# Optimization experiments

Hardware: AMD Instinct MI355X
Metric: run time of the kernel (lower is better)

## Reference

```python
import jax, jax.numpy as jnp
import numpy as np

D, N, M = 256, 8192, 8192
DISTANCE_THRESH = 0.8


def setup_inputs() -> dict:
    key = jax.random.key(0)
    k0, k1 = jax.random.split(key)
    d0 = jax.random.normal(k0, (D, N), dtype=jnp.float32)
    d1 = jax.random.normal(k1, (D, M), dtype=jnp.float32)
    # descriptors are L2-normalized along the feature dim (cosine similarity,
    # consistent with the 2*(1-sim) squared-distance formula in the module)
    d0 = d0 / jnp.linalg.norm(d0, axis=0, keepdims=True)
    d1 = d1 / jnp.linalg.norm(d1, axis=0, keepdims=True)
    return {"descriptors0": d0, "descriptors1": d1}


def reference(descriptors0, descriptors1):
    # nn_sim: [N, M] similarity matrix
    nn_sim = jnp.einsum('dn,dm->nm', descriptors0, descriptors1)
    nn_dist_01 = jnp.max(nn_sim, axis=1)          # [N]
    nn_idx_01 = jnp.argmax(nn_sim, axis=1)        # [N]
    nn_idx_10 = jnp.argmax(nn_sim, axis=0)        # [M]
    nn_dist = 2.0 * (1.0 - nn_dist_01)            # squared L2 dist for unit vecs
    ids1 = jnp.arange(nn_sim.shape[0])
    mask = ids1 == nn_idx_10[nn_idx_01]           # mutual NN check
    if DISTANCE_THRESH > 0.0:
        mask = mask & (nn_dist <= DISTANCE_THRESH ** 2)
    matches = jnp.where(mask, nn_idx_01, -1)
    scores = jnp.where(mask, (nn_dist + 1.0) / 2.0, 0.0)
    return matches, scores
```

## Files before the change

### kernel.cpp

```cpp
#include <hip/hip_runtime.h>
#include <hip/hip_bf16.h>

typedef __attribute__((ext_vector_type(8))) short short8;
typedef __attribute__((ext_vector_type(4))) float floatx4;
typedef unsigned int u32;

#define D_DIM 256
#define TCOLS 32
#define TILES 8
#define IDX_BITS 0x1FFFu
#define VAL_MASK 0xFFFFE000u


__device__ inline unsigned short f2bf_rne(float f) {
  u32 u = __float_as_uint(f);
  u32 r = (u + 0x7FFFu + ((u >> 16) & 1u)) >> 16;
  return (unsigned short)r;
}

__device__ inline u32 umax(u32 a, u32 b) { return a > b ? a : b; }

__device__ inline void async_ld16(const void* g, void* l) {
  __builtin_amdgcn_global_load_lds((const __attribute__((address_space(1))) void*)g,
                                   (__attribute__((address_space(3))) void*)l, 16, 0, 0);
}


__global__ __launch_bounds__(256) void transpose_cast(const float* __restrict__ src,
                                                      unsigned short* __restrict__ dst, int C,
                                                      u32* __restrict__ best, int init_n) {
  __shared__ alignas(16) unsigned short tile[64 * 132];
  const int tid = threadIdx.x;
  const int d = tid & 63;
  const int gd0 = blockIdx.x * 64;
  const int fy = blockIdx.y;
#pragma unroll
  for (int k = 0; k < 32; ++k) {
    int fl = (tid >> 6) + 4 * k;
    float v = src[(size_t)(fy * 128 + fl) * C + gd0 + d];
    tile[d * 132 + fl] = f2bf_rne(v);
  }
  __syncthreads();
#pragma unroll
  for (int c = 0; c < 4; ++c) {
    int slot = c * 256 + tid;
    int dd = slot >> 4, f8 = slot & 15;
    short8 o = *(const short8*)(tile + dd * 132 + f8 * 8);
    *(short8*)(dst + (size_t)(gd0 + dd) * D_DIM + fy * 128 + f8 * 8) = o;
  }
  if (fy == 0) {
    int i = blockIdx.x * 256 + tid;
    if (i < init_n) best[i] = 0u;
  }
}

template <bool PRECAST>
__global__ __launch_bounds__(256, 1) void gemm_reduce(const float* __restrict__ A,
                                                      const unsigned short* __restrict__ At,
                                                      const unsigned short* __restrict__ Bt,
                                                      u32* __restrict__ best01,
                                                      u32* __restrict__ best10,
                                                      int N) {
  __shared__ alignas(16) unsigned short sB[2][TCOLS * D_DIM];
  __shared__ u32 colbest[TILES * TCOLS];

  const int tid  = threadIdx.x;
  const int wave = tid >> 6;
  const int lane = tid & 63;
  const int quad = lane >> 4;
  const int l15  = lane & 15;
  const int n0   = blockIdx.x * 256;
  const int mg0  = blockIdx.y * (TILES * TCOLS);
  const int rbase = n0 + wave * 64;

  colbest[tid] = 0u;

  {
    const unsigned short* src = Bt + (size_t)mg0 * D_DIM;
#pragma unroll
    for (int c = 0; c < 4; ++c) {
      int slot = c * 256 + tid;
      int r = slot >> 5, cc = slot & 31;
      int ccg = (cc & 24) | ((cc ^ r) & 7);
      async_ld16(src + (size_t)r * D_DIM + ccg * 8, (unsigned short*)sB[0] + slot * 8);
    }
  }

  short8 af[4][8];
  if constexpr (PRECAST) {
#pragma unroll
    for (int t = 0; t < 4; ++t) {
      const unsigned short* ap = At + (size_t)(rbase + t * 16 + l15) * D_DIM + quad * 8;
#pragma unroll
      for (int kc = 0; kc < 8; ++kc)
        af[t][kc] = *(const short8*)(ap + kc * 32);
    }
  } else {
#pragma unroll
    for (int t = 0; t < 4; ++t)
#pragma unroll
      for (int kc = 0; kc < 8; ++kc) {
        const int row = rbase + t * 16 + l15;
        const int kb = kc * 32 + quad * 8;
        short8 o;
#pragma unroll
        for (int u = 0; u < 8; ++u)
          o[u] = (short)f2bf_rne(A[(size_t)(kb + u) * N + row]);
        af[t][kc] = o;
      }
  }

  u32 rbk[16];
  u32 rowpay[16];
#pragma unroll
  for (int i = 0; i < 4; ++i)
#pragma unroll
    for (int r = 0; r < 4; ++r) {
      rbk[i * 4 + r] = 0u;
      rowpay[i * 4 + r] = (~(u32)(rbase + i * 16 + quad * 4 + r)) & IDX_BITS;
    }

  __syncthreads();

  for (int mt = 0; mt < TILES; ++mt) {
    const int m0 = mg0 + mt * TCOLS;
    if (mt + 1 < TILES) {
      const unsigned short* src = Bt + (size_t)(m0 + TCOLS) * D_DIM;
      unsigned short* dstb = (unsigned short*)sB[(mt + 1) & 1];
#pragma unroll
      for (int c = 0; c < 4; ++c) {
        int slot = c * 256 + tid;
        int r = slot >> 5, cc = slot & 31;
        int ccg = (cc & 24) | ((cc ^ r) & 7);
        async_ld16(src + (size_t)r * D_DIM + ccg * 8, dstb + slot * 8);
      }
    }

    floatx4 acc[4][2];
#pragma unroll
    for (int i = 0; i < 4; ++i)
#pragma unroll
      for (int j = 0; j < 2; ++j)
        acc[i][j] = (floatx4){2.0f, 2.0f, 2.0f, 2.0f};

    const unsigned short* sb = (const unsigned short*)sB[mt & 1];
#pragma unroll
    for (int kc = 0; kc < 8; ++kc) {
      short8 bfr[2];
#pragma unroll
      for (int j = 0; j < 2; ++j) {
        int c2 = j * 16 + l15;
        int ch = kc * 4 + quad;
        int chg = (ch & 24) | ((ch ^ c2) & 7);
        bfr[j] = *(const short8*)(sb + c2 * D_DIM + chg * 8);
      }
#pragma unroll
      for (int i = 0; i < 4; ++i)
#pragma unroll
        for (int j = 0; j < 2; ++j)
          acc[i][j] = __builtin_amdgcn_mfma_f32_16x16x32_bf16(af[i][kc], bfr[j], acc[i][j], 0, 0, 0);
    }

    u32 cb[2] = {0u, 0u};
    u32 colpay[2];
#pragma unroll
    for (int j = 0; j < 2; ++j) colpay[j] = (~(u32)(m0 + j * 16 + l15)) & IDX_BITS;
#pragma unroll
    for (int i = 0; i < 4; ++i)
#pragma unroll
      for (int r = 0; r < 4; ++r) {
        u32 rp = rowpay[i * 4 + r];
        u32 rb = rbk[i * 4 + r];
#pragma unroll
        for (int j = 0; j < 2; ++j) {
          u32 u = __float_as_uint(acc[i][j][r]) & VAL_MASK;
          rb = umax(rb, u | colpay[j]);
          cb[j] = umax(cb[j], u | rp);
        }
        rbk[i * 4 + r] = rb;
      }
#pragma unroll
    for (int j = 0; j < 2; ++j) {
      u32 b = cb[j];
      b = umax(b, (u32)__shfl_xor((int)b, 16, 64));
      b = umax(b, (u32)__shfl_xor((int)b, 32, 64));
      if (quad == 0) atomicMax(&colbest[mt * TCOLS + j * 16 + l15], b);
    }
    __syncthreads();
  }

#pragma unroll
  for (int i = 0; i < 4; ++i)
#pragma unroll
    for (int r = 0; r < 4; ++r) {
      u32 b = rbk[i * 4 + r];
      b = umax(b, (u32)__shfl_xor((int)b, 1, 64));
      b = umax(b, (u32)__shfl_xor((int)b, 2, 64));
      b = umax(b, (u32)__shfl_xor((int)b, 4, 64));
      b = umax(b, (u32)__shfl_xor((int)b, 8, 64));
      if (l15 == 0) atomicMax(&best01[rbase + i * 16 + quad * 4 + r], b);
    }

  atomicMax(&best10[mg0 + tid], colbest[tid]);
}

__global__ void finalize(const u32* __restrict__ best01, const u32* __restrict__ best10,
                         float* __restrict__ out, int N) {
  int n = blockIdx.x * blockDim.x + threadIdx.x;
  if (n >= N) return;
  u32 k = best01[n];
  int idx01 = (int)((~k) & IDX_BITS);
  float sim = __uint_as_float(k & VAL_MASK) - 2.0f;
  int idx10 = (int)((~best10[idx01]) & IDX_BITS);
  float dist = 2.0f - 2.0f * sim;
  bool ok = (idx10 == n) && (dist <= 0.64f);
  out[n]     = ok ? (float)idx01 : -1.0f;
  out[N + n] = ok ? 1.5f - sim : 0.0f;
}


extern "C" void kernel_launch(void* const* d_in, const int* in_sizes, int n_in,
                              void* d_out, int out_size, void* d_ws, size_t ws_size,
                              hipStream_t stream) {
  (void)n_in; (void)out_size;
  const float* d0 = (const float*)d_in[0];
  const float* d1 = (const float*)d_in[1];
  const int N = in_sizes[0] / D_DIM;
  const int M = in_sizes[1] / D_DIM;

  u32* best01 = (u32*)d_ws;
  u32* best10 = best01 + N;
  unsigned short* At = (unsigned short*)(best10 + M);
  unsigned short* Bt = At + (size_t)N * D_DIM;
  float* out = (float*)d_out;

  const size_t need = (size_t)(N + M) * sizeof(u32) +
                      (size_t)(N + M) * D_DIM * sizeof(unsigned short);

  if (ws_size >= need) {
    hipLaunchKernelGGL(transpose_cast, dim3(N / 64, 2), dim3(256), 0, stream,
                       d0, At, N, best01, N + M);
    hipLaunchKernelGGL(transpose_cast, dim3(M / 64, 2), dim3(256), 0, stream,
                       d1, Bt, M, best01, 0);
    hipLaunchKernelGGL((gemm_reduce<true>), dim3(N / 256, M / (TILES * TCOLS)), dim3(256),
                       0, stream, d0, At, Bt, best01, best10, N);
  } else {
    unsigned short* BtF = (unsigned short*)(best10 + M);
    hipLaunchKernelGGL(transpose_cast, dim3(M / 64, 2), dim3(256), 0, stream,
                       d1, BtF, M, best01, N + M);
    hipLaunchKernelGGL((gemm_reduce<false>), dim3(N / 256, M / (TILES * TCOLS)), dim3(256),
                       0, stream, d0, BtF, BtF, best01, best10, N);
  }
  hipLaunchKernelGGL(finalize, dim3(N / 256), dim3(256), 0, stream, best01, best10, out, N);
}
```

Before: 114.1 us.

## Triple-buffer B tiles and overlap epilogue with next tile's MFMA

Switches the GEMM's B staging from double to triple buffering so two tiles are in flight, and replaces __syncthreads with explicit vmcnt waits plus s_barrier. The argmax epilogue of tile mt-1 now runs after tile mt's MFMAs, using two alternating accumulator sets, and MFMA sections are wrapped in s_setprio. The two transpose/cast launches are merged into one kernel, and row payloads are computed from a single base value to save registers. This aims to hide load latency and epilogue ALU work behind matrix ops. The cost is more LDS and a second accumulator set, which adds register pressure at one wave per SIMD.

```diff
diff --git a/kernel.cpp b/kernel.cpp
--- a/kernel.cpp
+++ b/kernel.cpp
@@ -25,14 +25,63 @@
                                    (__attribute__((address_space(3))) void*)l, 16, 0, 0);
 }
 
-
-__global__ __launch_bounds__(256) void transpose_cast(const float* __restrict__ src,
-                                                      unsigned short* __restrict__ dst, int C,
-                                                      u32* __restrict__ best, int init_n) {
+__device__ __forceinline__ void stage_tile(const unsigned short* __restrict__ src,
+                                           unsigned short* dstb, int tid) {
+#pragma unroll
+  for (int c = 0; c < 4; ++c) {
+    int slot = c * 256 + tid;
+    int r = slot >> 5, cc = slot & 31;
+    int ccg = (cc & 24) | ((cc ^ r) & 7);
+    async_ld16(src + (size_t)r * D_DIM + ccg * 8, dstb + slot * 8);
+  }
+}
+
+__device__ __forceinline__ void epilogue(const floatx4 (&acc)[4][2], int m0,
+                                         u32 (&rbk)[16], u32 rp0,
+                                         u32* __restrict__ colbest_tile,
+                                         int l15, int quad) {
+  u32 cb[2] = {0u, 0u};
+  u32 colpay[2] = {0x1FFFu - (u32)(m0 + l15), 0x1FFFu - (u32)(m0 + 16 + l15)};
+#pragma unroll
+  for (int i = 0; i < 4; ++i)
+#pragma unroll
+    for (int r = 0; r < 4; ++r) {
+      u32 rp = rp0 - (u32)(i * 16 + r);
+      u32 rb = rbk[i * 4 + r];
+#pragma unroll
+      for (int j = 0; j < 2; ++j) {
+        u32 u = __float_as_uint(acc[i][j][r]) & VAL_MASK;
+        rb = umax(rb, u | colpay[j]);
+        cb[j] = umax(cb[j], u | rp);
+      }
+      rbk[i * 4 + r] = rb;
+    }
+#pragma unroll
+  for (int j = 0; j < 2; ++j) {
+    u32 b = cb[j];
+    b = umax(b, (u32)__shfl_xor((int)b, 16, 64));
+    b = umax(b, (u32)__shfl_xor((int)b, 32, 64));
+    if (quad == 0) atomicMax(&colbest_tile[j * 16 + l15], b);
+  }
+}
+
+
+__global__ __launch_bounds__(256) void transpose_cast2(const float* __restrict__ d0,
+                                                       const float* __restrict__ d1,
+                                                       unsigned short* __restrict__ At,
+                                                       unsigned short* __restrict__ Bt,
+                                                       int N, int M,
+                                                       u32* __restrict__ best, int init_n) {
   __shared__ alignas(16) unsigned short tile[64 * 132];
   const int tid = threadIdx.x;
+  const int bx = blockIdx.x;
+  const int nblkA = N / 64;
+  const float* src;
+  unsigned short* dst;
+  int C, gd0;
+  if (bx < nblkA) { src = d0; dst = At; C = N; gd0 = bx * 64; }
+  else           { src = d1; dst = Bt; C = M; gd0 = (bx - nblkA) * 64; }
   const int d = tid & 63;
-  const int gd0 = blockIdx.x * 64;
   const int fy = blockIdx.y;
 #pragma unroll
   for (int k = 0; k < 32; ++k) {
@@ -49,7 +98,7 @@
     *(short8*)(dst + (size_t)(gd0 + dd) * D_DIM + fy * 128 + f8 * 8) = o;
   }
   if (fy == 0) {
-    int i = blockIdx.x * 256 + tid;
+    int i = bx * 256 + tid;
     if (i < init_n) best[i] = 0u;
   }
 }
@@ -61,7 +110,7 @@
                                                       u32* __restrict__ best01,
                                                       u32* __restrict__ best10,
                                                       int N) {
-  __shared__ alignas(16) unsigned short sB[2][TCOLS * D_DIM];
+  __shared__ alignas(16) unsigned short sB[3][TCOLS * D_DIM];
   __shared__ u32 colbest[TILES * TCOLS];
 
   const int tid  = threadIdx.x;
@@ -75,17 +124,6 @@
 
   colbest[tid] = 0u;
 
-  {
-    const unsigned short* src = Bt + (size_t)mg0 * D_DIM;
-#pragma unroll
-    for (int c = 0; c < 4; ++c) {
-      int slot = c * 256 + tid;
-      int r = slot >> 5, cc = slot & 31;
-      int ccg = (cc & 24) | ((cc ^ r) & 7);
-      async_ld16(src + (size_t)r * D_DIM + ccg * 8, (unsigned short*)sB[0] + slot * 8);
-    }
-  }
-
   short8 af[4][8];
   if constexpr (PRECAST) {
 #pragma unroll
@@ -110,40 +148,35 @@
       }
   }
 
+  stage_tile(Bt + (size_t)mg0 * D_DIM, (unsigned short*)sB[0], tid);
+  stage_tile(Bt + (size_t)(mg0 + TCOLS) * D_DIM, (unsigned short*)sB[1], tid);
+
   u32 rbk[16];
-  u32 rowpay[16];
-#pragma unroll
-  for (int i = 0; i < 4; ++i)
-#pragma unroll
-    for (int r = 0; r < 4; ++r) {
-      rbk[i * 4 + r] = 0u;
-      rowpay[i * 4 + r] = (~(u32)(rbase + i * 16 + quad * 4 + r)) & IDX_BITS;
-    }
-
-  __syncthreads();
-
+#pragma unroll
+  for (int s = 0; s < 16; ++s) rbk[s] = 0u;
+  const u32 rp0 = 0x1FFFu - (u32)(rbase + quad * 4);
+
+  asm volatile("s_waitcnt vmcnt(4)" ::: "memory");
+  __builtin_amdgcn_s_barrier();
+
+  floatx4 accA[4][2], accB[4][2];
+
+#pragma unroll
   for (int mt = 0; mt < TILES; ++mt) {
-    const int m0 = mg0 + mt * TCOLS;
-    if (mt + 1 < TILES) {
-      const unsigned short* src = Bt + (size_t)(m0 + TCOLS) * D_DIM;
-      unsigned short* dstb = (unsigned short*)sB[(mt + 1) & 1];
-#pragma unroll
-      for (int c = 0; c < 4; ++c) {
-        int slot = c * 256 + tid;
-        int r = slot >> 5, cc = slot & 31;
-        int ccg = (cc & 24) | ((cc ^ r) & 7);
-        async_ld16(src + (size_t)r * D_DIM + ccg * 8, dstb + slot * 8);
-      }
-    }
-
-    floatx4 acc[4][2];
+    if (mt + 2 < TILES)
+      stage_tile(Bt + (size_t)(mg0 + (mt + 2) * TCOLS) * D_DIM,
+                 (unsigned short*)sB[(mt + 2) % 3], tid);
+
+    floatx4 (&cur)[4][2] = (mt & 1) ? accB : accA;
+    floatx4 (&prv)[4][2] = (mt & 1) ? accA : accB;
 #pragma unroll
     for (int i = 0; i < 4; ++i)
 #pragma unroll
       for (int j = 0; j < 2; ++j)
-        acc[i][j] = (floatx4){2.0f, 2.0f, 2.0f, 2.0f};
-
-    const unsigned short* sb = (const unsigned short*)sB[mt & 1];
+        cur[i][j] = (floatx4){2.0f, 2.0f, 2.0f, 2.0f};
+
+    const unsigned short* sb = (const unsigned short*)sB[mt % 3];
+    __builtin_amdgcn_s_setprio(1);
 #pragma unroll
     for (int kc = 0; kc < 8; ++kc) {
       short8 bfr[2];
@@ -158,36 +191,24 @@
       for (int i = 0; i < 4; ++i)
 #pragma unroll
         for (int j = 0; j < 2; ++j)
-          acc[i][j] = __builtin_amdgcn_mfma_f32_16x16x32_bf16(af[i][kc], bfr[j], acc[i][j], 0, 0, 0);
-    }
-
-    u32 cb[2] = {0u, 0u};
-    u32 colpay[2];
-#pragma unroll
-    for (int j = 0; j < 2; ++j) colpay[j] = (~(u32)(m0 + j * 16 + l15)) & IDX_BITS;
-#pragma unroll
-    for (int i = 0; i < 4; ++i)
-#pragma unroll
-      for (int r = 0; r < 4; ++r) {
-        u32 rp = rowpay[i * 4 + r];
-        u32 rb = rbk[i * 4 + r];
-#pragma unroll
-        for (int j = 0; j < 2; ++j) {
-          u32 u = __float_as_uint(acc[i][j][r]) & VAL_MASK;
-          rb = umax(rb, u | colpay[j]);
-          cb[j] = umax(cb[j], u | rp);
-        }
-        rbk[i * 4 + r] = rb;
-      }
-#pragma unroll
-    for (int j = 0; j < 2; ++j) {
-      u32 b = cb[j];
-      b = umax(b, (u32)__shfl_xor((int)b, 16, 64));
-      b = umax(b, (u32)__shfl_xor((int)b, 32, 64));
-      if (quad == 0) atomicMax(&colbest[mt * TCOLS + j * 16 + l15], b);
-    }
-    __syncthreads();
-  }
+          cur[i][j] = __builtin_amdgcn_mfma_f32_16x16x32_bf16(af[i][kc], bfr[j], cur[i][j], 0, 0, 0);
+    }
+    __builtin_amdgcn_s_setprio(0);
+
+    if (mt > 0)
+      epilogue(prv, mg0 + (mt - 1) * TCOLS, rbk, rp0, &colbest[(mt - 1) * TCOLS], l15, quad);
+
+    if (mt + 1 < TILES) {
+      if (mt + 2 < TILES) {
+        asm volatile("s_waitcnt vmcnt(4)" ::: "memory");
+      } else {
+        asm volatile("s_waitcnt vmcnt(0)" ::: "memory");
+      }
+      __builtin_amdgcn_s_barrier();
+    }
+  }
+
+  epilogue(accB, mg0 + (TILES - 1) * TCOLS, rbk, rp0, &colbest[(TILES - 1) * TCOLS], l15, quad);
 
 #pragma unroll
   for (int i = 0; i < 4; ++i)
@@ -201,6 +222,8 @@
       if (l15 == 0) atomicMax(&best01[rbase + i * 16 + quad * 4 + r], b);
     }
 
+  asm volatile("s_waitcnt lgkmcnt(0)" ::: "memory");
+  __builtin_amdgcn_s_barrier();
   atomicMax(&best10[mg0 + tid], colbest[tid]);
 }
 
@@ -238,16 +261,14 @@
                       (size_t)(N + M) * D_DIM * sizeof(unsigned short);
 
   if (ws_size >= need) {
-    hipLaunchKernelGGL(transpose_cast, dim3(N / 64, 2), dim3(256), 0, stream,
-                       d0, At, N, best01, N + M);
-    hipLaunchKernelGGL(transpose_cast, dim3(M / 64, 2), dim3(256), 0, stream,
-                       d1, Bt, M, best01, 0);
+    hipLaunchKernelGGL(transpose_cast2, dim3((N + M) / 64, 2), dim3(256), 0, stream,
+                       d0, d1, At, Bt, N, M, best01, N + M);
     hipLaunchKernelGGL((gemm_reduce<true>), dim3(N / 256, M / (TILES * TCOLS)), dim3(256),
                        0, stream, d0, At, Bt, best01, best10, N);
   } else {
     unsigned short* BtF = (unsigned short*)(best10 + M);
-    hipLaunchKernelGGL(transpose_cast, dim3(M / 64, 2), dim3(256), 0, stream,
-                       d1, BtF, M, best01, N + M);
+    hipLaunchKernelGGL(transpose_cast2, dim3(M / 64, 2), dim3(256), 0, stream,
+                       d1, d1, BtF, BtF, M, M, best01, N + M);
     hipLaunchKernelGGL((gemm_reduce<false>), dim3(N / 256, M / (TILES * TCOLS)), dim3(256),
                        0, stream, d0, BtF, BtF, best01, best10, N);
   }
```

Measured after the change: 136.0 us. +19.2%, slower.

## Halve GEMM row tile, raise occupancy, merge transpose launches

Applied to the files above, without the earlier changes.

Each wave of the GEMM-reduce kernel now covers 32 rows instead of 64. That halves the A-fragment and accumulator registers, and the launch bound goes from 1 to 4 blocks per CU, with twice as many blocks in the grid. The two transpose/cast launches are merged into one kernel that splits on block index, saving a launch. Row payloads are computed on the fly rather than held in a register array. Each B tile staged through LDS is now reused across fewer rows, so LDS and global traffic for B roughly double in exchange for higher occupancy.

```diff
diff --git a/kernel.cpp b/kernel.cpp
--- a/kernel.cpp
+++ b/kernel.cpp
@@ -26,13 +26,22 @@
 }
 
 
-__global__ __launch_bounds__(256) void transpose_cast(const float* __restrict__ src,
-                                                      unsigned short* __restrict__ dst, int C,
-                                                      u32* __restrict__ best, int init_n) {
+__global__ __launch_bounds__(256) void transpose_cast2(const float* __restrict__ d0,
+                                                       const float* __restrict__ d1,
+                                                       unsigned short* __restrict__ At,
+                                                       unsigned short* __restrict__ Bt,
+                                                       int N, int M,
+                                                       u32* __restrict__ best, int init_n) {
   __shared__ alignas(16) unsigned short tile[64 * 132];
   const int tid = threadIdx.x;
+  const int bx = blockIdx.x;
+  const int nblkA = N / 64;
+  const float* src;
+  unsigned short* dst;
+  int C, gd0;
+  if (bx < nblkA) { src = d0; dst = At; C = N; gd0 = bx * 64; }
+  else           { src = d1; dst = Bt; C = M; gd0 = (bx - nblkA) * 64; }
   const int d = tid & 63;
-  const int gd0 = blockIdx.x * 64;
   const int fy = blockIdx.y;
 #pragma unroll
   for (int k = 0; k < 32; ++k) {
@@ -49,13 +58,13 @@
     *(short8*)(dst + (size_t)(gd0 + dd) * D_DIM + fy * 128 + f8 * 8) = o;
   }
   if (fy == 0) {
-    int i = blockIdx.x * 256 + tid;
+    int i = bx * 256 + tid;
     if (i < init_n) best[i] = 0u;
   }
 }
 
 template <bool PRECAST>
-__global__ __launch_bounds__(256, 1) void gemm_reduce(const float* __restrict__ A,
+__global__ __launch_bounds__(256, 4) void gemm_reduce(const float* __restrict__ A,
                                                       const unsigned short* __restrict__ At,
                                                       const unsigned short* __restrict__ Bt,
                                                       u32* __restrict__ best01,
@@ -69,9 +78,9 @@
   const int lane = tid & 63;
   const int quad = lane >> 4;
   const int l15  = lane & 15;
-  const int n0   = blockIdx.x * 256;
+  const int n0   = blockIdx.x * 128;
   const int mg0  = blockIdx.y * (TILES * TCOLS);
-  const int rbase = n0 + wave * 64;
+  const int rbase = n0 + wave * 32;
 
   colbest[tid] = 0u;
 
@@ -86,10 +95,10 @@
     }
   }
 
-  short8 af[4][8];
+  short8 af[2][8];
   if constexpr (PRECAST) {
 #pragma unroll
-    for (int t = 0; t < 4; ++t) {
+    for (int t = 0; t < 2; ++t) {
       const unsigned short* ap = At + (size_t)(rbase + t * 16 + l15) * D_DIM + quad * 8;
 #pragma unroll
       for (int kc = 0; kc < 8; ++kc)
@@ -97,7 +106,7 @@
     }
   } else {
 #pragma unroll
-    for (int t = 0; t < 4; ++t)
+    for (int t = 0; t < 2; ++t)
 #pragma unroll
       for (int kc = 0; kc < 8; ++kc) {
         const int row = rbase + t * 16 + l15;
@@ -110,15 +119,10 @@
       }
   }
 
-  u32 rbk[16];
-  u32 rowpay[16];
-#pragma unroll
-  for (int i = 0; i < 4; ++i)
-#pragma unroll
-    for (int r = 0; r < 4; ++r) {
-      rbk[i * 4 + r] = 0u;
-      rowpay[i * 4 + r] = (~(u32)(rbase + i * 16 + quad * 4 + r)) & IDX_BITS;
-    }
+  u32 rbk[8];
+#pragma unroll
+  for (int s = 0; s < 8; ++s) rbk[s] = 0u;
+  const u32 rp0 = 0x1FFFu - (u32)(rbase + quad * 4);
 
   __syncthreads();
 
@@ -136,9 +140,9 @@
       }
     }
 
-    floatx4 acc[4][2];
-#pragma unroll
-    for (int i = 0; i < 4; ++i)
+    floatx4 acc[2][2];
+#pragma unroll
+    for (int i = 0; i < 2; ++i)
 #pragma unroll
       for (int j = 0; j < 2; ++j)
         acc[i][j] = (floatx4){2.0f, 2.0f, 2.0f, 2.0f};
@@ -155,21 +159,19 @@
         bfr[j] = *(const short8*)(sb + c2 * D_DIM + chg * 8);
       }
 #pragma unroll
-      for (int i = 0; i < 4; ++i)
+      for (int i = 0; i < 2; ++i)
 #pragma unroll
         for (int j = 0; j < 2; ++j)
           acc[i][j] = __builtin_amdgcn_mfma_f32_16x16x32_bf16(af[i][kc], bfr[j], acc[i][j], 0, 0, 0);
     }
 
     u32 cb[2] = {0u, 0u};
-    u32 colpay[2];
-#pragma unroll
-    for (int j = 0; j < 2; ++j) colpay[j] = (~(u32)(m0 + j * 16 + l15)) & IDX_BITS;
-#pragma unroll
-    for (int i = 0; i < 4; ++i)
+    u32 colpay[2] = {0x1FFFu - (u32)(m0 + l15), 0x1FFFu - (u32)(m0 + 16 + l15)};
+#pragma unroll
+    for (int i = 0; i < 2; ++i)
 #pragma unroll
       for (int r = 0; r < 4; ++r) {
-        u32 rp = rowpay[i * 4 + r];
+        u32 rp = rp0 - (u32)(i * 16 + r);
         u32 rb = rbk[i * 4 + r];
 #pragma unroll
         for (int j = 0; j < 2; ++j) {
@@ -190,7 +192,7 @@
   }
 
 #pragma unroll
-  for (int i = 0; i < 4; ++i)
+  for (int i = 0; i < 2; ++i)
 #pragma unroll
     for (int r = 0; r < 4; ++r) {
       u32 b = rbk[i * 4 + r];
@@ -238,17 +240,15 @@
                       (size_t)(N + M) * D_DIM * sizeof(unsigned short);
 
   if (ws_size >= need) {
-    hipLaunchKernelGGL(transpose_cast, dim3(N / 64, 2), dim3(256), 0, stream,
-                       d0, At, N, best01, N + M);
-    hipLaunchKernelGGL(transpose_cast, dim3(M / 64, 2), dim3(256), 0, stream,
-                       d1, Bt, M, best01, 0);
-    hipLaunchKernelGGL((gemm_reduce<true>), dim3(N / 256, M / (TILES * TCOLS)), dim3(256),
+    hipLaunchKernelGGL(transpose_cast2, dim3((N + M) / 64, 2), dim3(256), 0, stream,
+                       d0, d1, At, Bt, N, M, best01, N + M);
+    hipLaunchKernelGGL((gemm_reduce<true>), dim3(N / 128, M / (TILES * TCOLS)), dim3(256),
                        0, stream, d0, At, Bt, best01, best10, N);
   } else {
     unsigned short* BtF = (unsigned short*)(best10 + M);
-    hipLaunchKernelGGL(transpose_cast, dim3(M / 64, 2), dim3(256), 0, stream,
-                       d1, BtF, M, best01, N + M);
-    hipLaunchKernelGGL((gemm_reduce<false>), dim3(N / 256, M / (TILES * TCOLS)), dim3(256),
+    hipLaunchKernelGGL(transpose_cast2, dim3(M / 64, 2), dim3(256), 0, stream,
+                       d1, d1, BtF, BtF, M, M, best01, N + M);
+    hipLaunchKernelGGL((gemm_reduce<false>), dim3(N / 128, M / (TILES * TCOLS)), dim3(256),
                        0, stream, d0, BtF, BtF, best01, best10, N);
   }
   hipLaunchKernelGGL(finalize, dim3(N / 256), dim3(256), 0, stream, best01, best10, out, N);
```

Result: slower. 188.9 us (+65.5%).

## Load B fragments directly from pre-swizzled global layout, dropping LDS staging

Applied to the files above, without the earlier changes.

The transpose kernel now writes descriptors1 in an MFMA-fragment-ordered layout, so each lane can load its B operand directly from global memory (through L2) into registers with software prefetch. This removes LDS double-buffering and the per-tile block barriers. It also fuses the two transpose launches into one, switches to a 1D grid with an XCD-aware block remap, and raises launch bounds to two blocks per CU. The cost is more global/L2 traffic per wave, since every wave reloads the same B tile, and higher register pressure from the prefetched fragments.

```diff
diff --git a/kernel.cpp b/kernel.cpp
--- a/kernel.cpp
+++ b/kernel.cpp
@@ -20,19 +20,22 @@
 
 __device__ inline u32 umax(u32 a, u32 b) { return a > b ? a : b; }
 
-__device__ inline void async_ld16(const void* g, void* l) {
-  __builtin_amdgcn_global_load_lds((const __attribute__((address_space(1))) void*)g,
-                                   (__attribute__((address_space(3))) void*)l, 16, 0, 0);
-}
-
-
-__global__ __launch_bounds__(256) void transpose_cast(const float* __restrict__ src,
-                                                      unsigned short* __restrict__ dst, int C,
-                                                      u32* __restrict__ best, int init_n) {
+
+__global__ __launch_bounds__(256) void transpose_cast2(const float* __restrict__ d0,
+                                                       const float* __restrict__ d1,
+                                                       unsigned short* __restrict__ At,
+                                                       unsigned short* __restrict__ Bt2,
+                                                       int N, int M,
+                                                       u32* __restrict__ best, int init_n) {
   __shared__ alignas(16) unsigned short tile[64 * 132];
   const int tid = threadIdx.x;
+  const int bx = blockIdx.x;
+  const int nblkA = N / 64;
+  const bool isA = bx < nblkA;
+  const float* src = isA ? d0 : d1;
+  const int C = isA ? N : M;
+  const int gd0 = (isA ? bx : bx - nblkA) * 64;
   const int d = tid & 63;
-  const int gd0 = blockIdx.x * 64;
   const int fy = blockIdx.y;
 #pragma unroll
   for (int k = 0; k < 32; ++k) {
@@ -41,27 +44,40 @@
     tile[d * 132 + fl] = f2bf_rne(v);
   }
   __syncthreads();
-#pragma unroll
-  for (int c = 0; c < 4; ++c) {
-    int slot = c * 256 + tid;
-    int dd = slot >> 4, f8 = slot & 15;
-    short8 o = *(const short8*)(tile + dd * 132 + f8 * 8);
-    *(short8*)(dst + (size_t)(gd0 + dd) * D_DIM + fy * 128 + f8 * 8) = o;
+  if (isA) {
+#pragma unroll
+    for (int c = 0; c < 4; ++c) {
+      int slot = c * 256 + tid;
+      int dd = slot >> 4, f8 = slot & 15;
+      short8 o = *(const short8*)(tile + dd * 132 + f8 * 8);
+      *(short8*)(At + (size_t)(gd0 + dd) * D_DIM + fy * 128 + f8 * 8) = o;
+    }
+  } else {
+#pragma unroll
+    for (int c = 0; c < 4; ++c) {
+      int slot = c * 256 + tid;
+      int dd = slot & 63;
+      int f8l = c * 4 + (tid >> 6);
+      int f8g = fy * 16 + f8l;
+      short8 o = *(const short8*)(tile + dd * 132 + f8l * 8);
+      size_t off = (size_t)((gd0 + dd) >> 5) * 8192 + (size_t)(f8g >> 2) * 1024 +
+                   (size_t)((dd >> 4) & 1) * 512 + (f8g & 3) * 128 + (dd & 15) * 8;
+      *(short8*)(Bt2 + off) = o;
+    }
   }
   if (fy == 0) {
-    int i = blockIdx.x * 256 + tid;
+    int i = bx * 256 + tid;
     if (i < init_n) best[i] = 0u;
   }
 }
 
 template <bool PRECAST>
-__global__ __launch_bounds__(256, 1) void gemm_reduce(const float* __restrict__ A,
+__global__ __launch_bounds__(256, 2) void gemm_reduce(const float* __restrict__ A,
                                                       const unsigned short* __restrict__ At,
-                                                      const unsigned short* __restrict__ Bt,
+                                                      const unsigned short* __restrict__ Bt2,
                                                       u32* __restrict__ best01,
                                                       u32* __restrict__ best10,
-                                                      int N) {
-  __shared__ alignas(16) unsigned short sB[2][TCOLS * D_DIM];
+                                                      int N, int M) {
   __shared__ u32 colbest[TILES * TCOLS];
 
   const int tid  = threadIdx.x;
@@ -69,22 +85,23 @@
   const int lane = tid & 63;
   const int quad = lane >> 4;
   const int l15  = lane & 15;
-  const int n0   = blockIdx.x * 256;
-  const int mg0  = blockIdx.y * (TILES * TCOLS);
+
+  const int xB = N >> 8, yB = M >> 8;
+  const int bid = blockIdx.x;
+  int x, y;
+  if ((yB & 7) == 0) {
+    int c = bid & 7, k = bid >> 3;
+    x = k % xB;
+    y = c * (yB >> 3) + k / xB;
+  } else {
+    x = bid % xB;
+    y = bid / xB;
+  }
+  const int n0  = x * 256;
+  const int mg0 = y * (TILES * TCOLS);
   const int rbase = n0 + wave * 64;
 
   colbest[tid] = 0u;
-
-  {
-    const unsigned short* src = Bt + (size_t)mg0 * D_DIM;
-#pragma unroll
-    for (int c = 0; c < 4; ++c) {
-      int slot = c * 256 + tid;
-      int r = slot >> 5, cc = slot & 31;
-      int ccg = (cc & 24) | ((cc ^ r) & 7);
-      async_ld16(src + (size_t)r * D_DIM + ccg * 8, (unsigned short*)sB[0] + slot * 8);
-    }
-  }
 
   short8 af[4][8];
   if constexpr (PRECAST) {
@@ -110,32 +127,24 @@
       }
   }
 
+  const unsigned short* bp = Bt2 + (size_t)(mg0 >> 5) * 8192 + (size_t)lane * 8;
+
+  short8 bfA[4][2];
+#pragma unroll
+  for (int kc = 0; kc < 4; ++kc)
+#pragma unroll
+    for (int j = 0; j < 2; ++j)
+      bfA[kc][j] = *(const short8*)(bp + (kc * 2 + j) * 512);
+
   u32 rbk[16];
-  u32 rowpay[16];
-#pragma unroll
-  for (int i = 0; i < 4; ++i)
-#pragma unroll
-    for (int r = 0; r < 4; ++r) {
-      rbk[i * 4 + r] = 0u;
-      rowpay[i * 4 + r] = (~(u32)(rbase + i * 16 + quad * 4 + r)) & IDX_BITS;
-    }
+#pragma unroll
+  for (int s = 0; s < 16; ++s) rbk[s] = 0u;
+  const u32 rp0 = 0x1FFFu - (u32)(rbase + quad * 4);
 
   __syncthreads();
 
   for (int mt = 0; mt < TILES; ++mt) {
-    const int m0 = mg0 + mt * TCOLS;
-    if (mt + 1 < TILES) {
-      const unsigned short* src = Bt + (size_t)(m0 + TCOLS) * D_DIM;
-      unsigned short* dstb = (unsigned short*)sB[(mt + 1) & 1];
-#pragma unroll
-      for (int c = 0; c < 4; ++c) {
-        int slot = c * 256 + tid;
-        int r = slot >> 5, cc = slot & 31;
-        int ccg = (cc & 24) | ((cc ^ r) & 7);
-        async_ld16(src + (size_t)r * D_DIM + ccg * 8, dstb + slot * 8);
-      }
-    }
-
+    const unsigned short* bpt = bp + (size_t)mt * 8192;
     floatx4 acc[4][2];
 #pragma unroll
     for (int i = 0; i < 4; ++i)
@@ -143,33 +152,44 @@
       for (int j = 0; j < 2; ++j)
         acc[i][j] = (floatx4){2.0f, 2.0f, 2.0f, 2.0f};
 
-    const unsigned short* sb = (const unsigned short*)sB[mt & 1];
-#pragma unroll
-    for (int kc = 0; kc < 8; ++kc) {
-      short8 bfr[2];
-#pragma unroll
-      for (int j = 0; j < 2; ++j) {
-        int c2 = j * 16 + l15;
-        int ch = kc * 4 + quad;
-        int chg = (ch & 24) | ((ch ^ c2) & 7);
-        bfr[j] = *(const short8*)(sb + c2 * D_DIM + chg * 8);
-      }
+#pragma unroll
+    for (int kc = 0; kc < 4; ++kc)
 #pragma unroll
       for (int i = 0; i < 4; ++i)
 #pragma unroll
         for (int j = 0; j < 2; ++j)
-          acc[i][j] = __builtin_amdgcn_mfma_f32_16x16x32_bf16(af[i][kc], bfr[j], acc[i][j], 0, 0, 0);
-    }
-
+          acc[i][j] = __builtin_amdgcn_mfma_f32_16x16x32_bf16(af[i][kc], bfA[kc][j], acc[i][j], 0, 0, 0);
+
+#pragma unroll
+    for (int kc = 0; kc < 4; ++kc)
+#pragma unroll
+      for (int j = 0; j < 2; ++j)
+        bfA[kc][j] = *(const short8*)(bpt + ((kc + 4) * 2 + j) * 512);
+
+#pragma unroll
+    for (int kc = 0; kc < 4; ++kc)
+#pragma unroll
+      for (int i = 0; i < 4; ++i)
+#pragma unroll
+        for (int j = 0; j < 2; ++j)
+          acc[i][j] = __builtin_amdgcn_mfma_f32_16x16x32_bf16(af[i][kc + 4], bfA[kc][j], acc[i][j], 0, 0, 0);
+
+    if (mt + 1 < TILES) {
+#pragma unroll
+      for (int kc = 0; kc < 4; ++kc)
+#pragma unroll
+        for (int j = 0; j < 2; ++j)
+          bfA[kc][j] = *(const short8*)(bpt + 8192 + (kc * 2 + j) * 512);
+    }
+
+    const int m0 = mg0 + mt * TCOLS;
     u32 cb[2] = {0u, 0u};
-    u32 colpay[2];
-#pragma unroll
-    for (int j = 0; j < 2; ++j) colpay[j] = (~(u32)(m0 + j * 16 + l15)) & IDX_BITS;
+    u32 colpay[2] = {0x1FFFu - (u32)(m0 + l15), 0x1FFFu - (u32)(m0 + 16 + l15)};
 #pragma unroll
     for (int i = 0; i < 4; ++i)
 #pragma unroll
       for (int r = 0; r < 4; ++r) {
-        u32 rp = rowpay[i * 4 + r];
+        u32 rp = rp0 - (u32)(i * 16 + r);
         u32 rb = rbk[i * 4 + r];
 #pragma unroll
         for (int j = 0; j < 2; ++j) {
@@ -186,7 +206,6 @@
       b = umax(b, (u32)__shfl_xor((int)b, 32, 64));
       if (quad == 0) atomicMax(&colbest[mt * TCOLS + j * 16 + l15], b);
     }
-    __syncthreads();
   }
 
 #pragma unroll
@@ -201,6 +220,7 @@
       if (l15 == 0) atomicMax(&best01[rbase + i * 16 + quad * 4 + r], b);
     }
 
+  __syncthreads();
   atomicMax(&best10[mg0 + tid], colbest[tid]);
 }
 
@@ -230,26 +250,25 @@
 
   u32* best01 = (u32*)d_ws;
   u32* best10 = best01 + N;
-  unsigned short* At = (unsigned short*)(best10 + M);
-  unsigned short* Bt = At + (size_t)N * D_DIM;
+  unsigned short* At  = (unsigned short*)(best10 + M);
+  unsigned short* Bt2 = At + (size_t)N * D_DIM;
   float* out = (float*)d_out;
 
+  const int nBlocks = (N / 256) * (M / 256);
   const size_t need = (size_t)(N + M) * sizeof(u32) +
                       (size_t)(N + M) * D_DIM * sizeof(unsigned short);
 
   if (ws_size >= need) {
-    hipLaunchKernelGGL(transpose_cast, dim3(N / 64, 2), dim3(256), 0, stream,
-                       d0, At, N, best01, N + M);
-    hipLaunchKernelGGL(transpose_cast, dim3(M / 64, 2), dim3(256), 0, stream,
-                       d1, Bt, M, best01, 0);
-    hipLaunchKernelGGL((gemm_reduce<true>), dim3(N / 256, M / (TILES * TCOLS)), dim3(256),
-                       0, stream, d0, At, Bt, best01, best10, N);
+    hipLaunchKernelGGL(transpose_cast2, dim3((N + M) / 64, 2), dim3(256), 0, stream,
+                       d0, d1, At, Bt2, N, M, best01, N + M);
+    hipLaunchKernelGGL((gemm_reduce<true>), dim3(nBlocks), dim3(256), 0, stream,
+                       d0, At, Bt2, best01, best10, N, M);
   } else {
     unsigned short* BtF = (unsigned short*)(best10 + M);
-    hipLaunchKernelGGL(transpose_cast, dim3(M / 64, 2), dim3(256), 0, stream,
-                       d1, BtF, M, best01, N + M);
-    hipLaunchKernelGGL((gemm_reduce<false>), dim3(N / 256, M / (TILES * TCOLS)), dim3(256),
-                       0, stream, d0, BtF, BtF, best01, best10, N);
+    hipLaunchKernelGGL(transpose_cast2, dim3(M / 64, 2), dim3(256), 0, stream,
+                       d1, d1, BtF, BtF, 0, M, best01, N + M);
+    hipLaunchKernelGGL((gemm_reduce<false>), dim3(nBlocks), dim3(256), 0, stream,
+                       d0, BtF, BtF, best01, best10, N, M);
   }
   hipLaunchKernelGGL(finalize, dim3(N / 256), dim3(256), 0, stream, best01, best10, out, N);
 }
```

After: 114.3 us. Within noise of the previous version (+0.1%).
